# Kernel optimization log

Hardware: AMD Instinct MI355X
Metric: run time of the kernel (lower is better)

The kernel has to match this reference:

```python
import jax, jax.numpy as jnp
import numpy as np

DIM = 768
HEADS = 12
DH = DIM // HEADS
HID = 4 * DIM
EPS = 1e-5


def _layernorm(y, g, b):
    mu = jnp.mean(y, axis=-1, keepdims=True)
    var = jnp.mean(jnp.square(y - mu), axis=-1, keepdims=True)
    return (y - mu) * jax.lax.rsqrt(var + EPS) * g + b


def setup_inputs() -> dict:
    key = jax.random.key(0)
    ks = jax.random.split(key, 8)
    s = 0.02
    return {
        "x": jax.random.normal(ks[0], (8, 1024, DIM), dtype=jnp.float32),
        "Wqkv": jax.random.normal(ks[1], (DIM, 3 * DIM), dtype=jnp.float32) * s,
        "bqkv": jnp.zeros((3 * DIM,), jnp.float32),
        "Wproj": jax.random.normal(ks[2], (DIM, DIM), dtype=jnp.float32) * s,
        "bproj": jnp.zeros((DIM,), jnp.float32),
        "W1": jax.random.normal(ks[3], (DIM, HID), dtype=jnp.float32) * s,
        "b1": jnp.zeros((HID,), jnp.float32),
        "W2": jax.random.normal(ks[4], (HID, DIM), dtype=jnp.float32) * s,
        "b2": jnp.zeros((DIM,), jnp.float32),
        "g1": jnp.ones((DIM,), jnp.float32),
        "be1": jnp.zeros((DIM,), jnp.float32),
        "g2": jnp.ones((DIM,), jnp.float32),
        "be2": jnp.zeros((DIM,), jnp.float32),
    }


def reference(x, Wqkv, bqkv, Wproj, bproj, W1, b1, W2, b2, g1, be1, g2, be2):
    b, n, d = x.shape
    # QKV projection; source splits last dim as (h, d_head, qkv) -> qkv innermost
    qkv = (x @ Wqkv + bqkv).reshape(b, n, HEADS, DH, 3)
    q, k, v = qkv[..., 0], qkv[..., 1], qkv[..., 2]  # [b, n, h, dh]
    scores = jnp.einsum('bqhd,bkhd->bhqk', q, k)
    # NOTE: source applies the 1/sqrt(dim) scale AFTER softmax (quirk preserved)
    attn = jax.nn.softmax(scores, axis=-1) / (d ** 0.5)
    out = jnp.einsum('bhqk,bkhd->bqhd', attn, v).reshape(b, n, d)
    attn_out = out @ Wproj + bproj
    # Residual with norm on the branch output (not pre-norm), per source
    x = x + _layernorm(attn_out, g1, be1)
    mlp_out = jax.nn.gelu(x @ W1 + b1, approximate=False) @ W2 + b2
    return x + _layernorm(mlp_out, g2, be2)
```

## Files before the change

### kernel.cpp

```cpp
#include <hip/hip_runtime.h>
#include <math.h>

typedef float f32x4 __attribute__((ext_vector_type(4)));
typedef short s16x8 __attribute__((ext_vector_type(8)));

#define DIM_ 768
#define HEADS_ 12
#define DH_ 64
#define HID_ 3072
#define SEQ_ 1024
#define BATCH_ 8
#define ROWS_ (BATCH_*SEQ_)

static __device__ __forceinline__ ushort f2bf(float f) {
    union { float f; unsigned u; } v; v.f = f;
    unsigned r = (v.u + 0x7fffu + ((v.u >> 16) & 1u)) >> 16;
    return (ushort)r;
}
static __device__ __forceinline__ float bf2f(ushort u) {
    union { unsigned u; float f; } v; v.u = ((unsigned)u) << 16;
    return v.f;
}

static __device__ __forceinline__ void glds16(const ushort* gp, ushort* lp) {
    __builtin_amdgcn_global_load_lds(
        (const __attribute__((address_space(1))) void*)gp,
        (__attribute__((address_space(3))) void*)lp, 16, 0, 0);
}

__global__ __launch_bounds__(256) void cast_bf16_kernel(
    const float* __restrict__ in, ushort* __restrict__ out, int n4)
{
    int i = blockIdx.x * 256 + threadIdx.x;
    if (i >= n4) return;
    float4 v = ((const float4*)in)[i];
    ushort4 o;
    o.x = f2bf(v.x); o.y = f2bf(v.y); o.z = f2bf(v.z); o.w = f2bf(v.w);
    ((ushort4*)out)[i] = o;
}

__global__ __launch_bounds__(256) void transpose_cast_kernel(
    const float* __restrict__ W, ushort* __restrict__ WT, int K, int N)
{
    __shared__ float tile[32][33];
    int n0 = blockIdx.x * 32, k0 = blockIdx.y * 32;
    int tx = threadIdx.x, ty = threadIdx.y;
#pragma unroll
    for (int i = 0; i < 4; i++)
        tile[ty + i * 8][tx] = W[(size_t)(k0 + ty + i * 8) * N + n0 + tx];
    __syncthreads();
#pragma unroll
    for (int i = 0; i < 4; i++)
        WT[(size_t)(n0 + ty + i * 8) * K + k0 + tx] = f2bf(tile[tx][ty + i * 8]);
}

__global__ __launch_bounds__(256) void transpose_cast_qkv_kernel(
    const float* __restrict__ W, ushort* __restrict__ WT)
{
    __shared__ float tile[32][33];
    int n0 = blockIdx.x * 32, k0 = blockIdx.y * 32;
    int tx = threadIdx.x, ty = threadIdx.y;
    int np = n0 + tx;
    int part = np / 768, idx = np % 768;
    int oc = ((idx >> 6) * 192) + ((idx & 63) * 3) + part;
#pragma unroll
    for (int i = 0; i < 4; i++)
        tile[ty + i * 8][tx] = W[(size_t)(k0 + ty + i * 8) * 2304 + oc];
    __syncthreads();
#pragma unroll
    for (int i = 0; i < 4; i++)
        WT[(size_t)(n0 + ty + i * 8) * 768 + k0 + tx] = f2bf(tile[tx][ty + i * 8]);
}

__global__ __launch_bounds__(256) void v_transpose_kernel(
    const ushort* __restrict__ vb, ushort* __restrict__ vT)
{
    __shared__ ushort tile[32][33];
    int dh0 = blockIdx.x * 32;
    int sq0 = blockIdx.y * 32;
    int bh  = blockIdx.z;
    int tx = threadIdx.x, ty = threadIdx.y;
    const ushort* src = vb + (size_t)bh * SEQ_ * DH_;
    ushort* dst = vT + (size_t)bh * DH_ * SEQ_;
#pragma unroll
    for (int i = 0; i < 4; i++)
        tile[ty + i * 8][tx] = src[(size_t)(sq0 + ty + i * 8) * DH_ + dh0 + tx];
    __syncthreads();
#pragma unroll
    for (int i = 0; i < 4; i++)
        dst[(size_t)(dh0 + ty + i * 8) * SEQ_ + sq0 + tx] = tile[tx][ty + i * 8];
}

#define EPI_PART 0
#define EPI_GELU 1
#define EPI_QKV 2

template<int EPI>
__global__ __launch_bounds__(256, 4) void gemm_bt(
    const ushort* __restrict__ A, const ushort* __restrict__ B,
    const float* __restrict__ bias,
    ushort* __restrict__ Cp,
    ushort* __restrict__ Qb, ushort* __restrict__ Kb, ushort* __restrict__ Vb,
    int M, int N, int K, int nx, int nk, int Ksl)
{
    __shared__ ushort As[128 * 64];
    __shared__ ushort Bs[128 * 64];
    const int t = threadIdx.x;
    const int lane = t & 63;
    const int w = t >> 6;
    const int wr = w >> 1, wc = w & 1;
    const int nwg = gridDim.x;
    const int chunk = nwg >> 3;
    const int lin = (blockIdx.x & 7) * chunk + (blockIdx.x >> 3);
    const int tile = lin / nk;
    const int ks = lin - tile * nk;
    const int m0 = (tile / nx) * 128, n0 = (tile % nx) * 128;
    const int lr = lane & 15, g = lane >> 4;

    const ushort* Ak = A + (size_t)ks * Ksl;
    const ushort* Bk = B + (size_t)ks * Ksl;
    const int sr = lane >> 3;
    const int scz = (((lane & 7) ^ sr)) * 8;

    f32x4 acc[4][4] = {};

    for (int k0 = 0; k0 < Ksl; k0 += 64) {
#pragma unroll
        for (int j = 0; j < 4; j++) {
            int r = w * 32 + j * 8;
            glds16(Ak + (size_t)(m0 + r + sr) * K + k0 + scz, &As[r * 64]);
            glds16(Bk + (size_t)(n0 + r + sr) * K + k0 + scz, &Bs[r * 64]);
        }
        __syncthreads();
#pragma unroll
        for (int kk = 0; kk < 2; kk++) {
            s16x8 af[4], bfr[4];
#pragma unroll
            for (int m = 0; m < 4; m++) {
                int row = wr * 64 + m * 16 + lr;
                int slot = (kk * 4 + g) ^ (row & 7);
                af[m] = *(const s16x8*)&As[row * 64 + slot * 8];
            }
#pragma unroll
            for (int n = 0; n < 4; n++) {
                int row = wc * 64 + n * 16 + lr;
                int slot = (kk * 4 + g) ^ (row & 7);
                bfr[n] = *(const s16x8*)&Bs[row * 64 + slot * 8];
            }
#pragma unroll
            for (int m = 0; m < 4; m++)
#pragma unroll
                for (int n = 0; n < 4; n++)
                    acc[m][n] = __builtin_amdgcn_mfma_f32_16x16x32_bf16(af[m], bfr[n], acc[m][n], 0, 0, 0);
        }
        __syncthreads();
    }

    ushort* Cpo = Cp ? Cp + (size_t)ks * M * N : nullptr;
    const int part = (EPI == EPI_QKV) ? (n0 / 768) : 0;
#pragma unroll
    for (int m = 0; m < 4; m++) {
        int row = m0 + wr * 64 + m * 16 + g * 4;
#pragma unroll
        for (int n = 0; n < 4; n++) {
            int col = n0 + wc * 64 + n * 16 + lr;
            float bv;
            int h = 0, dh = 0;
            if (EPI == EPI_QKV) {
                int idx = col - part * 768;
                h = idx >> 6; dh = idx & 63;
                bv = bias[h * 192 + dh * 3 + part];
            } else {
                bv = (ks == 0) ? bias[col] : 0.f;
            }
#pragma unroll
            for (int r = 0; r < 4; r++) {
                float v = acc[m][n][r] + bv;
                int rg = row + r;
                if (EPI == EPI_PART) {
                    Cpo[(size_t)rg * N + col] = f2bf(v);
                } else if (EPI == EPI_GELU) {
                    float u = v * (0.7978845608f + 0.0356774081f * v * v);
                    float th = 1.f - 2.f / (__expf(2.f * u) + 1.f);
                    float gl = 0.5f * v * (1.f + th);
                    Cpo[(size_t)rg * N + col] = f2bf(gl);
                } else {
                    int b = rg >> 10, nrow = rg & 1023;
                    int hb = b * HEADS_ + h;
                    ushort bw = f2bf(v);
                    ushort* dst = (part == 0) ? Qb : (part == 1) ? Kb : Vb;
                    dst[((size_t)hb * SEQ_ + nrow) * DH_ + dh] = bw;
                }
            }
        }
    }
}

static __device__ __forceinline__ void pack_pv(
    const f32x4 (&S)[4], s16x8& pf0v, s16x8& pf1v)
{
    unsigned c[4][2];
#pragma unroll
    for (int n = 0; n < 4; n++) {
        asm("v_cvt_pk_bf16_f32 %0, %1, %2" : "=v"(c[n][0]) : "v"(S[n][0]), "v"(S[n][1]));
        asm("v_cvt_pk_bf16_f32 %0, %1, %2" : "=v"(c[n][1]) : "v"(S[n][2]), "v"(S[n][3]));
    }
    union { unsigned u[4]; s16x8 v; } pf0, pf1;
#pragma unroll
    for (int m = 0; m < 2; m++) {
        unsigned a = c[0][m], bb = c[1][m];
        asm("v_permlane32_swap_b32 %0, %1" : "+v"(a), "+v"(bb));
        asm("v_permlane16_swap_b32 %0, %1" : "+v"(a), "+v"(bb));
        pf0.u[m] = a; pf0.u[2 + m] = bb;
        unsigned a2 = c[2][m], b2 = c[3][m];
        asm("v_permlane32_swap_b32 %0, %1" : "+v"(a2), "+v"(b2));
        asm("v_permlane16_swap_b32 %0, %1" : "+v"(a2), "+v"(b2));
        pf1.u[m] = a2; pf1.u[2 + m] = b2;
    }
    pf0v = pf0.v; pf1v = pf1.v;
}

struct AttnState {
    s16x8 aqA0, aqA1, aqB0, aqB1;
    float lA, lB;
    f32x4 OA[4], OB[4];
};

static __device__ __forceinline__ void attn_tile_lds(
    AttnState& st, const ushort* Ksb, const ushort* Vsb, int lr, int g)
{
    const float CMAX = 20.f;
    const int x = lr & 7;
    s16x8 kf[8], vf[8];
#pragma unroll
    for (int n = 0; n < 4; n++) {
        int row = n * 16 + lr;
        kf[2 * n]     = *(const s16x8*)&Ksb[row * 64 + (g ^ x) * 8];
        kf[2 * n + 1] = *(const s16x8*)&Ksb[row * 64 + ((4 + g) ^ x) * 8];
        vf[2 * n]     = *(const s16x8*)&Vsb[row * 64 + (g ^ x) * 8];
        vf[2 * n + 1] = *(const s16x8*)&Vsb[row * 64 + ((4 + g) ^ x) * 8];
    }
    f32x4 SA[4] = {}, SB[4] = {};
#pragma unroll
    for (int n = 0; n < 4; n++) {
        SA[n] = __builtin_amdgcn_mfma_f32_16x16x32_bf16(kf[2 * n], st.aqA0, SA[n], 0, 0, 0);
        SA[n] = __builtin_amdgcn_mfma_f32_16x16x32_bf16(kf[2 * n + 1], st.aqA1, SA[n], 0, 0, 0);
    }
#pragma unroll
    for (int n = 0; n < 4; n++) {
        SB[n] = __builtin_amdgcn_mfma_f32_16x16x32_bf16(kf[2 * n], st.aqB0, SB[n], 0, 0, 0);
        SB[n] = __builtin_amdgcn_mfma_f32_16x16x32_bf16(kf[2 * n + 1], st.aqB1, SB[n], 0, 0, 0);
    }
#pragma unroll
    for (int n = 0; n < 4; n++)
#pragma unroll
        for (int r = 0; r < 4; r++) {
            SA[n][r] = __expf(SA[n][r] - CMAX);
            SB[n][r] = __expf(SB[n][r] - CMAX);
        }
    f32x4 sa = SA[0] + SA[1], sb = SB[0] + SB[1];
    sa += SA[2] + SA[3];
    sb += SB[2] + SB[3];
    st.lA += (sa[0] + sa[1]) + (sa[2] + sa[3]);
    st.lB += (sb[0] + sb[1]) + (sb[2] + sb[3]);

    s16x8 pfA0, pfA1, pfB0, pfB1;
    pack_pv(SA, pfA0, pfA1);
    pack_pv(SB, pfB0, pfB1);

#pragma unroll
    for (int n = 0; n < 4; n++) {
        st.OA[n] = __builtin_amdgcn_mfma_f32_16x16x32_bf16(pfA0, vf[2 * n], st.OA[n], 0, 0, 0);
        st.OA[n] = __builtin_amdgcn_mfma_f32_16x16x32_bf16(pfA1, vf[2 * n + 1], st.OA[n], 0, 0, 0);
    }
#pragma unroll
    for (int n = 0; n < 4; n++) {
        st.OB[n] = __builtin_amdgcn_mfma_f32_16x16x32_bf16(pfB0, vf[2 * n], st.OB[n], 0, 0, 0);
        st.OB[n] = __builtin_amdgcn_mfma_f32_16x16x32_bf16(pfB1, vf[2 * n + 1], st.OB[n], 0, 0, 0);
    }
}

__global__ __launch_bounds__(256) void attn_kernel(
    const ushort* __restrict__ Q, const ushort* __restrict__ Kb,
    const ushort* __restrict__ Vt, ushort* __restrict__ AO)
{
    __shared__ ushort Ks[2][64 * 64];
    __shared__ ushort Vs[2][64 * 64];
    const int tid = threadIdx.x, lane = tid & 63, w = tid >> 6;
    const int lr = lane & 15, g = lane >> 4;
    const int wg = blockIdx.x;
    const int lin = (wg & 7) * 96 + (wg >> 3);
    const int bh = lin >> 3;
    const int qt = lin & 7;
    const int b = bh / HEADS_, h = bh % HEADS_;
    const ushort* qh = Q + (size_t)bh * SEQ_ * DH_;
    const ushort* kh = Kb + (size_t)bh * SEQ_ * DH_;
    const ushort* vh = Vt + (size_t)bh * DH_ * SEQ_;

    const int srow = tid >> 3;
    const int ss = (tid & 7) ^ (srow & 7);

    AttnState st;
    const int qbase = qt * 128 + w * 32;
    st.aqA0 = *(const s16x8*)(qh + (size_t)(qbase + lr) * DH_ + g * 8);
    st.aqA1 = *(const s16x8*)(qh + (size_t)(qbase + lr) * DH_ + 32 + g * 8);
    st.aqB0 = *(const s16x8*)(qh + (size_t)(qbase + 16 + lr) * DH_ + g * 8);
    st.aqB1 = *(const s16x8*)(qh + (size_t)(qbase + 16 + lr) * DH_ + 32 + g * 8);
    st.lA = 0.f; st.lB = 0.f;
#pragma unroll
    for (int n = 0; n < 4; n++) { st.OA[n] = f32x4{}; st.OB[n] = f32x4{}; }

    auto stageK = [&](ushort* buf, int kbase) {
        glds16(kh + (size_t)(kbase + srow) * DH_ + ss * 8, &buf[tid * 8]);
        glds16(kh + (size_t)(kbase + 32 + srow) * DH_ + ss * 8, &buf[tid * 8 + 2048]);
    };
    auto stageV = [&](ushort* buf, int kbase) {
        glds16(vh + (size_t)srow * SEQ_ + kbase + ss * 8, &buf[tid * 8]);
        glds16(vh + (size_t)(32 + srow) * SEQ_ + kbase + ss * 8, &buf[tid * 8 + 2048]);
    };

    stageK(Ks[0], 0);
    stageV(Vs[0], 0);
    __syncthreads();

#pragma unroll 1
    for (int tkv = 0; tkv < 16; tkv += 2) {
        if (tkv + 1 < 16) { stageK(Ks[1], (tkv + 1) * 64); stageV(Vs[1], (tkv + 1) * 64); }
        attn_tile_lds(st, Ks[0], Vs[0], lr, g);
        __syncthreads();
        if (tkv + 2 < 16) { stageK(Ks[0], (tkv + 2) * 64); stageV(Vs[0], (tkv + 2) * 64); }
        attn_tile_lds(st, Ks[1], Vs[1], lr, g);
        __syncthreads();
    }

    float lA = st.lA, lB = st.lB;
    lA += __shfl_xor(lA, 16); lA += __shfl_xor(lA, 32);
    lB += __shfl_xor(lB, 16); lB += __shfl_xor(lB, 32);

    const float fin = 0.03608439182435161f;
#pragma unroll
    for (int r = 0; r < 4; r++) {
        float linvA = fin / __shfl(lA, 4 * g + r);
        float linvB = fin / __shfl(lB, 4 * g + r);
        int rowA = b * SEQ_ + qbase + 4 * g + r;
        int rowB = rowA + 16;
        ushort* aoA = AO + (size_t)rowA * DIM_ + h * DH_ + lr;
        ushort* aoB = AO + (size_t)rowB * DIM_ + h * DH_ + lr;
#pragma unroll
        for (int n = 0; n < 4; n++) {
            aoA[n * 16] = f2bf(st.OA[n][r] * linvA);
            aoB[n * 16] = f2bf(st.OB[n][r] * linvB);
        }
    }
}

__global__ __launch_bounds__(256) void ln_residual_kernel(
    const float* __restrict__ xinf, const ushort* __restrict__ xinb,
    const ushort* __restrict__ y0, const ushort* __restrict__ y1,
    const float* __restrict__ g, const float* __restrict__ be,
    float* __restrict__ outf, ushort* __restrict__ outbf, int rows)
{
    int w = threadIdx.x >> 6, lane = threadIdx.x & 63;
    int row = blockIdx.x * 4 + w;
    if (row >= rows) return;
    const ushort4* y0r = (const ushort4*)(y0 + (size_t)row * DIM_);
    const ushort4* y1r = y1 ? (const ushort4*)(y1 + (size_t)row * DIM_) : nullptr;
    float4 v[3];
    float s = 0.f, s2 = 0.f;
#pragma unroll
    for (int i = 0; i < 3; i++) {
        ushort4 u0 = y0r[i * 64 + lane];
        float4 a = { bf2f(u0.x), bf2f(u0.y), bf2f(u0.z), bf2f(u0.w) };
        if (y1r) {
            ushort4 u1 = y1r[i * 64 + lane];
            a.x += bf2f(u1.x); a.y += bf2f(u1.y); a.z += bf2f(u1.z); a.w += bf2f(u1.w);
        }
        v[i] = a;
        s += (a.x + a.y) + (a.z + a.w);
        s2 += (a.x * a.x + a.y * a.y) + (a.z * a.z + a.w * a.w);
    }
#pragma unroll
    for (int o = 1; o < 64; o <<= 1) { s += __shfl_xor(s, o); s2 += __shfl_xor(s2, o); }
    float mu = s * (1.f / 768.f);
    float var = s2 * (1.f / 768.f) - mu * mu;
    float rs = rsqrtf(var + 1e-5f);
    const float4* xr = xinf ? (const float4*)(xinf + (size_t)row * DIM_) : nullptr;
    const ushort4* xb = xinb ? (const ushort4*)(xinb + (size_t)row * DIM_) : nullptr;
    const float4* g4 = (const float4*)g;
    const float4* b4 = (const float4*)be;
    float4* of = outf ? (float4*)(outf + (size_t)row * DIM_) : nullptr;
#pragma unroll
    for (int i = 0; i < 3; i++) {
        int c = i * 64 + lane;
        float4 gg = g4[c], bb = b4[c];
        float4 xx;
        if (xr) xx = xr[c];
        else {
            ushort4 u = xb[c];
            xx = { bf2f(u.x), bf2f(u.y), bf2f(u.z), bf2f(u.w) };
        }
        float4 o;
        o.x = xx.x + (v[i].x - mu) * rs * gg.x + bb.x;
        o.y = xx.y + (v[i].y - mu) * rs * gg.y + bb.y;
        o.z = xx.z + (v[i].z - mu) * rs * gg.z + bb.z;
        o.w = xx.w + (v[i].w - mu) * rs * gg.w + bb.w;
        if (of) of[c] = o;
        if (outbf) {
            ushort4 ob;
            ob.x = f2bf(o.x); ob.y = f2bf(o.y); ob.z = f2bf(o.z); ob.w = f2bf(o.w);
            ((ushort4*)(outbf + (size_t)row * DIM_))[c] = ob;
        }
    }
}

extern "C" void kernel_launch(void* const* d_in, const int* in_sizes, int n_in,
                              void* d_out, int out_size, void* d_ws, size_t ws_size,
                              hipStream_t stream)
{
    const float* x    = (const float*)d_in[0];
    const float* Wqkv = (const float*)d_in[1];
    const float* bqkv = (const float*)d_in[2];
    const float* Wproj= (const float*)d_in[3];
    const float* bproj= (const float*)d_in[4];
    const float* W1   = (const float*)d_in[5];
    const float* b1   = (const float*)d_in[6];
    const float* W2   = (const float*)d_in[7];
    const float* b2   = (const float*)d_in[8];
    const float* g1   = (const float*)d_in[9];
    const float* be1  = (const float*)d_in[10];
    const float* g2   = (const float*)d_in[11];
    const float* be2  = (const float*)d_in[12];
    float* out = (float*)d_out;

    char* ws = (char*)d_ws;
    size_t off = 0;
    auto alloc = [&](size_t bytes) -> void* {
        void* p = ws + off;
        off += (bytes + 255) & ~(size_t)255;
        return p;
    };
    ushort* wqkvT  = (ushort*)alloc((size_t)2304 * 768 * 2);
    ushort* wprojT = (ushort*)alloc((size_t)768 * 768 * 2);
    ushort* w1T    = (ushort*)alloc((size_t)3072 * 768 * 2);
    ushort* w2T    = (ushort*)alloc((size_t)768 * 3072 * 2);
    ushort* xbf    = (ushort*)alloc((size_t)ROWS_ * DIM_ * 2);
    ushort* qb     = (ushort*)alloc((size_t)ROWS_ * DIM_ * 2);
    ushort* kb     = (ushort*)alloc((size_t)ROWS_ * DIM_ * 2);
    ushort* vb     = (ushort*)alloc((size_t)ROWS_ * DIM_ * 2);
    ushort* hbf    = xbf;
    ushort* vT     = (ushort*)alloc((size_t)ROWS_ * DIM_ * 2);
    ushort* aobf   = (ushort*)alloc((size_t)ROWS_ * DIM_ * 2);
    ushort* projp  = (ushort*)alloc((size_t)2 * ROWS_ * DIM_ * 2);
    ushort* x1bf   = (ushort*)alloc((size_t)ROWS_ * DIM_ * 2);
    ushort* projp1 = projp + (size_t)ROWS_ * DIM_;

    cast_bf16_kernel<<<(ROWS_ * DIM_ / 4 + 255) / 256, 256, 0, stream>>>(x, xbf, ROWS_ * DIM_ / 4);
    transpose_cast_qkv_kernel<<<dim3(2304 / 32, 768 / 32), dim3(32, 8), 0, stream>>>(Wqkv, wqkvT);
    transpose_cast_kernel<<<dim3(768 / 32, 768 / 32), dim3(32, 8), 0, stream>>>(Wproj, wprojT, 768, 768);
    transpose_cast_kernel<<<dim3(3072 / 32, 768 / 32), dim3(32, 8), 0, stream>>>(W1, w1T, 768, 3072);
    transpose_cast_kernel<<<dim3(768 / 32, 3072 / 32), dim3(32, 8), 0, stream>>>(W2, w2T, 3072, 768);

    gemm_bt<EPI_QKV><<<1152, 256, 0, stream>>>(
        xbf, wqkvT, bqkv, nullptr, qb, kb, vb, ROWS_, 2304, 768, 18, 1, 768);

    v_transpose_kernel<<<dim3(2, 32, 96), dim3(32, 8), 0, stream>>>(vb, vT);

    attn_kernel<<<768, 256, 0, stream>>>(qb, kb, vT, aobf);

    gemm_bt<EPI_PART><<<768, 256, 0, stream>>>(
        aobf, wprojT, bproj, projp, nullptr, nullptr, nullptr, ROWS_, 768, 768, 6, 2, 384);

    ln_residual_kernel<<<ROWS_ / 4, 256, 0, stream>>>(
        x, nullptr, projp, projp1, g1, be1, nullptr, x1bf, ROWS_);

    gemm_bt<EPI_GELU><<<1536, 256, 0, stream>>>(
        x1bf, w1T, b1, hbf, nullptr, nullptr, nullptr, ROWS_, 3072, 768, 24, 1, 768);

    gemm_bt<EPI_PART><<<768, 256, 0, stream>>>(
        hbf, w2T, b2, projp, nullptr, nullptr, nullptr, ROWS_, 768, 3072, 6, 2, 1536);

    ln_residual_kernel<<<ROWS_ / 4, 256, 0, stream>>>(
        nullptr, x1bf, projp, projp1, g2, be2, out, nullptr, ROWS_);
}
```

Before: 240.6 us.

## Add 256x256-tile double-buffered GEMM for MLP layers with 4-way split-K

Introduces a new 512-thread GEMM kernel with 256x256 output tiles, double-buffered LDS staging, XOR-swizzled shared-memory layout, XCD-aware block remapping and interleaved MFMA phases. It is used for both MLP GEMMs, and the second MLP GEMM now splits K four ways instead of two. The layernorm-residual kernel is generalised to sum a variable number of partial buffers. The aim is more data reuse per tile and better overlap of loads with MFMA, at the cost of extra partial-sum traffic for the 4-way split and lower occupancy.

```diff
diff --git a/kernel.cpp b/kernel.cpp
--- a/kernel.cpp
+++ b/kernel.cpp
@@ -182,14 +182,131 @@
                 } else if (EPI == EPI_GELU) {
                     float u = v * (0.7978845608f + 0.0356774081f * v * v);
                     float th = 1.f - 2.f / (__expf(2.f * u) + 1.f);
-                    float gl = 0.5f * v * (1.f + th);
-                    Cpo[(size_t)rg * N + col] = f2bf(gl);
+                    Cpo[(size_t)rg * N + col] = f2bf(0.5f * v * (1.f + th));
                 } else {
                     int b = rg >> 10, nrow = rg & 1023;
                     int hb = b * HEADS_ + h;
                     ushort bw = f2bf(v);
                     ushort* dst = (part == 0) ? Qb : (part == 1) ? Kb : Vb;
                     dst[((size_t)hb * SEQ_ + nrow) * DH_ + dh] = bw;
+                }
+            }
+        }
+    }
+}
+
+template<int EPI>
+__global__ __launch_bounds__(512, 1) void gemm256(
+    const ushort* __restrict__ A, const ushort* __restrict__ B,
+    const float* __restrict__ bias, ushort* __restrict__ Cp,
+    int M, int N, int K, int nx, int nk, int Ksl)
+{
+    __shared__ ushort Abuf[2][2][128 * 64];
+    __shared__ ushort Bbuf[2][2][128 * 64];
+    const int tid = threadIdx.x;
+    const int lane = tid & 63, w = tid >> 6;
+    const int wm = w >> 2, wn = w & 3;
+    const int lr = lane & 15, g = lane >> 4;
+    const int nwg = gridDim.x, chunk = nwg >> 3;
+    const int lin = (blockIdx.x & 7) * chunk + (blockIdx.x >> 3);
+    const int tile = lin / nk, ks = lin - tile * nk;
+    const int m0 = (tile / nx) * 256, n0 = (tile % nx) * 256;
+    const ushort* Ak = A + (size_t)ks * Ksl;
+    const ushort* Bk = B + (size_t)ks * Ksl;
+    const int nt = Ksl >> 6;
+
+    const int srw = lane >> 3;
+    const int ssl = (lane & 7) ^ (lane >> 3);
+
+    auto stageHalf = [&](int buf, int kt, int hid) {
+        const ushort* src = (hid < 2) ? Ak : Bk;
+        const int base = (hid < 2) ? m0 : n0;
+        const int half = hid & 1;
+        ushort* dst = (hid < 2) ? &Abuf[buf][half][0] : &Bbuf[buf][half][0];
+#pragma unroll
+        for (int j = 0; j < 2; j++) {
+            int brow = (w * 2 + j) * 8;
+            glds16(src + (size_t)(base + half * 128 + brow + srw) * K + kt * 64 + ssl * 8,
+                   &dst[brow * 64]);
+        }
+    };
+
+    f32x4 acc[8][4] = {};
+    s16x8 bfr[8];
+
+#pragma unroll
+    for (int h = 0; h < 4; h++) stageHalf(0, 0, h);
+
+    const int niter = nt >> 1;
+    for (int s = 0; s < niter; ++s) {
+#pragma unroll
+        for (int p = 0; p < 8; p++) {
+            const int q = p & 3, bufc = p >> 2;
+            const int skt = (p < 4) ? (2 * s + 1) : (2 * s + 2);
+            const int sbuf = (p < 4) ? 1 : 0;
+            const bool do_stage = (skt < nt);
+            if (do_stage) stageHalf(sbuf, skt, q);
+            if (q == 0) {
+                if (do_stage) asm volatile("s_waitcnt vmcnt(2)" ::: "memory");
+                else          asm volatile("s_waitcnt vmcnt(0)" ::: "memory");
+            }
+            __builtin_amdgcn_s_barrier();
+            __builtin_amdgcn_sched_barrier(0);
+            if (q == 0) {
+                const ushort* bb = &Bbuf[bufc][wn >> 1][0];
+                const int rl = (wn & 1) * 64;
+#pragma unroll
+                for (int ni = 0; ni < 4; ni++)
+#pragma unroll
+                    for (int kk = 0; kk < 2; kk++) {
+                        int row = rl + ni * 16 + lr;
+                        int slot = (kk * 4 + g) ^ (row & 7);
+                        bfr[ni * 2 + kk] = *(const s16x8*)&bb[row * 64 + slot * 8];
+                    }
+            }
+            s16x8 af[4];
+            const ushort* ab = &Abuf[bufc][wm][0];
+#pragma unroll
+            for (int m2 = 0; m2 < 2; m2++)
+#pragma unroll
+                for (int kk = 0; kk < 2; kk++) {
+                    int row = (2 * q + m2) * 16 + lr;
+                    int slot = (kk * 4 + g) ^ (row & 7);
+                    af[m2 * 2 + kk] = *(const s16x8*)&ab[row * 64 + slot * 8];
+                }
+            __builtin_amdgcn_s_setprio(1);
+#pragma unroll
+            for (int m2 = 0; m2 < 2; m2++)
+#pragma unroll
+                for (int ni = 0; ni < 4; ni++)
+#pragma unroll
+                    for (int kk = 0; kk < 2; kk++)
+                        acc[2 * q + m2][ni] = __builtin_amdgcn_mfma_f32_16x16x32_bf16(
+                            af[m2 * 2 + kk], bfr[ni * 2 + kk], acc[2 * q + m2][ni], 0, 0, 0);
+            __builtin_amdgcn_s_setprio(0);
+            __builtin_amdgcn_s_barrier();
+            __builtin_amdgcn_sched_barrier(0);
+        }
+    }
+
+    ushort* Cpo = Cp + (size_t)ks * M * N;
+#pragma unroll
+    for (int mi = 0; mi < 8; mi++) {
+        int row = m0 + wm * 128 + mi * 16 + g * 4;
+#pragma unroll
+        for (int ni = 0; ni < 4; ni++) {
+            int col = n0 + wn * 64 + ni * 16 + lr;
+            float bv = (ks == 0) ? bias[col] : 0.f;
+#pragma unroll
+            for (int r = 0; r < 4; r++) {
+                float v = acc[mi][ni][r] + bv;
+                int rg = row + r;
+                if (EPI == EPI_GELU) {
+                    float u = v * (0.7978845608f + 0.0356774081f * v * v);
+                    float th = 1.f - 2.f / (__expf(2.f * u) + 1.f);
+                    Cpo[(size_t)rg * N + col] = f2bf(0.5f * v * (1.f + th));
+                } else {
+                    Cpo[(size_t)rg * N + col] = f2bf(v);
                 }
             }
         }
@@ -356,24 +473,22 @@
 
 __global__ __launch_bounds__(256) void ln_residual_kernel(
     const float* __restrict__ xinf, const ushort* __restrict__ xinb,
-    const ushort* __restrict__ y0, const ushort* __restrict__ y1,
+    const ushort* __restrict__ y, int np,
     const float* __restrict__ g, const float* __restrict__ be,
     float* __restrict__ outf, ushort* __restrict__ outbf, int rows)
 {
     int w = threadIdx.x >> 6, lane = threadIdx.x & 63;
     int row = blockIdx.x * 4 + w;
     if (row >= rows) return;
-    const ushort4* y0r = (const ushort4*)(y0 + (size_t)row * DIM_);
-    const ushort4* y1r = y1 ? (const ushort4*)(y1 + (size_t)row * DIM_) : nullptr;
+    const size_t pstride = (size_t)ROWS_ * DIM_;
     float4 v[3];
     float s = 0.f, s2 = 0.f;
 #pragma unroll
     for (int i = 0; i < 3; i++) {
-        ushort4 u0 = y0r[i * 64 + lane];
-        float4 a = { bf2f(u0.x), bf2f(u0.y), bf2f(u0.z), bf2f(u0.w) };
-        if (y1r) {
-            ushort4 u1 = y1r[i * 64 + lane];
-            a.x += bf2f(u1.x); a.y += bf2f(u1.y); a.z += bf2f(u1.z); a.w += bf2f(u1.w);
+        float4 a = { 0.f, 0.f, 0.f, 0.f };
+        for (int j = 0; j < np; j++) {
+            ushort4 u = ((const ushort4*)(y + j * pstride + (size_t)row * DIM_))[i * 64 + lane];
+            a.x += bf2f(u.x); a.y += bf2f(u.y); a.z += bf2f(u.z); a.w += bf2f(u.w);
         }
         v[i] = a;
         s += (a.x + a.y) + (a.z + a.w);
@@ -450,9 +565,8 @@
     ushort* hbf    = xbf;
     ushort* vT     = (ushort*)alloc((size_t)ROWS_ * DIM_ * 2);
     ushort* aobf   = (ushort*)alloc((size_t)ROWS_ * DIM_ * 2);
-    ushort* projp  = (ushort*)alloc((size_t)2 * ROWS_ * DIM_ * 2);
+    ushort* projp  = (ushort*)alloc((size_t)4 * ROWS_ * DIM_ * 2);
     ushort* x1bf   = (ushort*)alloc((size_t)ROWS_ * DIM_ * 2);
-    ushort* projp1 = projp + (size_t)ROWS_ * DIM_;
 
     cast_bf16_kernel<<<(ROWS_ * DIM_ / 4 + 255) / 256, 256, 0, stream>>>(x, xbf, ROWS_ * DIM_ / 4);
     transpose_cast_qkv_kernel<<<dim3(2304 / 32, 768 / 32), dim3(32, 8), 0, stream>>>(Wqkv, wqkvT);
@@ -471,14 +585,14 @@
         aobf, wprojT, bproj, projp, nullptr, nullptr, nullptr, ROWS_, 768, 768, 6, 2, 384);
 
     ln_residual_kernel<<<ROWS_ / 4, 256, 0, stream>>>(
-        x, nullptr, projp, projp1, g1, be1, nullptr, x1bf, ROWS_);
-
-    gemm_bt<EPI_GELU><<<1536, 256, 0, stream>>>(
-        x1bf, w1T, b1, hbf, nullptr, nullptr, nullptr, ROWS_, 3072, 768, 24, 1, 768);
-
-    gemm_bt<EPI_PART><<<768, 256, 0, stream>>>(
-        hbf, w2T, b2, projp, nullptr, nullptr, nullptr, ROWS_, 768, 3072, 6, 2, 1536);
+        x, nullptr, projp, 2, g1, be1, nullptr, x1bf, ROWS_);
+
+    gemm256<EPI_GELU><<<384, 512, 0, stream>>>(
+        x1bf, w1T, b1, hbf, ROWS_, 3072, 768, 12, 1, 768);
+
+    gemm256<EPI_PART><<<384, 512, 0, stream>>>(
+        hbf, w2T, b2, projp, ROWS_, 768, 3072, 3, 4, 768);
 
     ln_residual_kernel<<<ROWS_ / 4, 256, 0, stream>>>(
-        nullptr, x1bf, projp, projp1, g2, be2, out, nullptr, ROWS_);
-}
+        nullptr, x1bf, projp, 4, g2, be2, out, nullptr, ROWS_);
+}
```

New measurement: 301.7 us. +25.4%, slower.
